# Performance work log

Hardware: AMD Instinct MI355X
Metric: run time of the kernel (lower is better)

The kernel has to match this reference:

```python
import jax, jax.numpy as jnp
import numpy as np

B, N, D = 4, 1024, 512
H, Dv, Dq = 8, 64, 64
NUM_BUCKETS = 64
LN_EPS = 1e-5


def setup_inputs() -> dict:
    key = jax.random.key(0)
    ks = jax.random.split(key, 10)
    x = jax.random.normal(ks[0], (B, N, D), dtype=jnp.float32)
    ts = jnp.sort(jax.random.randint(ks[1], (B, N), 0, 1_000_000), axis=1).astype(jnp.int64)
    cm = jnp.triu(jnp.ones((N, N), dtype=bool), k=1)  # causal: mask j > i
    pm = jnp.zeros((B, N), dtype=bool)                # no padding
    uvqk = 0.02 * jax.random.normal(ks[2], (D, 2 * H * Dv + 2 * H * Dq), dtype=jnp.float32)
    lim = float(np.sqrt(6.0 / (H * Dv + D)))
    o_w = jax.random.uniform(ks[3], (H * Dv, D), minval=-lim, maxval=lim, dtype=jnp.float32)
    o_b = jnp.zeros((D,), dtype=jnp.float32)
    ln_x_w = jnp.ones((D,), jnp.float32); ln_x_b = jnp.zeros((D,), jnp.float32)
    ln_a_w = jnp.ones((H * Dv,), jnp.float32); ln_a_b = jnp.zeros((H * Dv,), jnp.float32)
    ts_w = 0.02 * jax.random.normal(ks[4], (NUM_BUCKETS + 1,), dtype=jnp.float32)
    pos_w = 0.02 * jax.random.normal(ks[5], (2 * N - 1,), dtype=jnp.float32)
    return {"x": x, "ts": ts, "cm": cm, "pm": pm, "uvqk": uvqk, "o_w": o_w, "o_b": o_b,
            "ln_x_w": ln_x_w, "ln_x_b": ln_x_b, "ln_a_w": ln_a_w, "ln_a_b": ln_a_b,
            "ts_w": ts_w, "pos_w": pos_w}


def _layernorm(x, w, b):
    m = jnp.mean(x, axis=-1, keepdims=True)
    v = jnp.mean(jnp.square(x - m), axis=-1, keepdims=True)
    return (x - m) / jnp.sqrt(v + LN_EPS) * w + b


def _rel_bias(ts, ts_w, pos_w):
    # positional part: pb[i, j] = pos_w[j - i + N - 1], shape [N, N]
    idx = jnp.arange(N)
    pb = pos_w[idx[None, :] - idx[:, None] + N - 1]
    # bucketed time part
    ext = jnp.concatenate([ts, ts[:, N - 1:N]], axis=1)           # [B, N+1]
    diff = ext[:, 1:, None] - ext[:, None, :-1]                   # [B, N, N]
    logd = jnp.log(jnp.maximum(jnp.abs(diff), 1).astype(jnp.float32))
    bk = jnp.clip((logd / 0.301).astype(jnp.int32), 0, NUM_BUCKETS)
    return pb[None] + ts_w[bk]                                    # [B, N, N]


def reference(x, ts, cm, pm, uvqk, o_w, o_b, ln_x_w, ln_x_b, ln_a_w, ln_a_b, ts_w, pos_w):
    nx = _layernorm(x, ln_x_w, ln_x_b)                            # [B, N, D]
    out = jax.nn.silu(jnp.einsum('bnd,de->bne', nx, uvqk))        # [B, N, 2HDv+2HDq]
    u, v, q, k = jnp.split(out, [H * Dv, 2 * H * Dv, 2 * H * Dv + H * Dq], axis=-1)
    q = q.reshape(B, N, H, Dq)
    k = k.reshape(B, N, H, Dq)
    v = v.reshape(B, N, H, Dv)
    qk = jnp.einsum('bihd,bjhd->bhij', q, k) + _rel_bias(ts, ts_w, pos_w)[:, None]
    qk = jax.nn.silu(qk) / N
    qk = jnp.where(cm[None, None], 0.0, qk)          # causal mask
    qk = jnp.where(pm[:, None, None, :], 0.0, qk)    # padding mask on keys
    ao = jnp.einsum('bhij,bjhd->bihd', qk, v).reshape(B, N, H * Dv)
    ao = _layernorm(ao, ln_a_w, ln_a_b)
    u = u.reshape(B, N, H * Dv)
    y = (u * ao) @ o_w + o_b + x
    return jnp.where(pm[:, :, None], 0.0, y)
```

## Files before the change

### kernel.cpp

```cpp
#include <hip/hip_runtime.h>
#include <hip/hip_bf16.h>


typedef __attribute__((ext_vector_type(8))) short short8;
typedef __attribute__((ext_vector_type(4))) short bf4;
typedef __attribute__((ext_vector_type(4))) float floatx4;
typedef __attribute__((ext_vector_type(16))) float floatx16;

#define MFMA_BF16 __builtin_amdgcn_mfma_f32_16x16x32_bf16
#define MFMA32 __builtin_amdgcn_mfma_f32_32x32x16_bf16

static __device__ __forceinline__ short f2bf(float f) {
  unsigned u = __builtin_bit_cast(unsigned, f);
  u = (u + 0x7fffu + ((u >> 16) & 1u)) >> 16;
  return (short)u;
}
static __device__ __forceinline__ unsigned pk_bf16(float a, float b) {
  __hip_bfloat162 h = __float22bfloat162_rn(float2{a, b});
  unsigned u;
  __builtin_memcpy(&u, &h, 4);
  return u;
}
static __device__ __forceinline__ short lo16(unsigned u) { return (short)(u & 0xffffu); }
static __device__ __forceinline__ short hi16(unsigned u) { return (short)(u >> 16); }
static __device__ __forceinline__ float bf2f(short s) {
  unsigned u = ((unsigned)(unsigned short)s) << 16;
  return __builtin_bit_cast(float, u);
}
static __device__ __forceinline__ float bflo(unsigned u) {
  return __builtin_bit_cast(float, u << 16);
}
static __device__ __forceinline__ float bfhi(unsigned u) {
  return __builtin_bit_cast(float, u & 0xffff0000u);
}
static __device__ __forceinline__ float silu_f(float x) {
  return x / (1.f + __expf(-x));
}
static __device__ __forceinline__ void permswap(unsigned& a, unsigned& b) {
#if __has_builtin(__builtin_amdgcn_permlane32_swap)
  typedef __attribute__((ext_vector_type(2))) unsigned uint2v;
  uint2v r = __builtin_amdgcn_permlane32_swap(a, b, false, false);
  a = r[0];
  b = r[1];
#else
  asm volatile("v_permlane32_swap_b32 %0, %1" : "+v"(a), "+v"(b));
#endif
}
static __device__ __forceinline__ short8 mk8(unsigned a, unsigned b, unsigned c,
                                             unsigned d) {
  union {
    unsigned u[4];
    short8 s;
  } r;
  r.u[0] = a;
  r.u[1] = b;
  r.u[2] = c;
  r.u[3] = d;
  return r.s;
}
static __device__ __forceinline__ void gl_lds16(const void* g, void* l) {
  __builtin_amdgcn_global_load_lds(
      (const __attribute__((address_space(1))) unsigned int*)g,
      (__attribute__((address_space(3))) unsigned int*)l, 16, 0, 0);
}

__global__ __launch_bounds__(256) void prep_kernel(
    const float* __restrict__ x, const int* __restrict__ ts,
    const float* __restrict__ uvqk, const float* __restrict__ o_w,
    const float* __restrict__ ln_x_w, const float* __restrict__ ln_x_b,
    const float* __restrict__ ts_w, const float* __restrict__ pos_w,
    short* __restrict__ nx, short* __restrict__ uvqk_t,
    short* __restrict__ o_wt, short* __restrict__ bias) {
  __shared__ float tile[32][33];
  const int id = blockIdx.x;
  const int t = threadIdx.x;
  if (id < 4096) {
    const int b = id >> 10, i = id & 1023;
    int ie = i + 1; if (ie > 1023) ie = 1023;
    const int tse = ts[(b << 10) + ie];
    const int j0 = t * 4;
    int4 tj = *(const int4*)&ts[(b << 10) + j0];
    const int* tjp = (const int*)&tj;
    float ov[4];
#pragma unroll
    for (int e = 0; e < 4; ++e) {
      int dt = tse - tjp[e];
      float ad = fabsf((float)dt);
      if (ad < 1.f) ad = 1.f;
      int bkt = (int)(__logf(ad) * (1.f / 0.301f));
      if (bkt > 64) bkt = 64;
      ov[e] = pos_w[j0 + e - i + 1023] + ts_w[bkt];
    }
    uint2 o2 = {pk_bf16(ov[0], ov[1]), pk_bf16(ov[2], ov[3])};
    *(uint2*)&bias[((size_t)id << 10) + j0] = o2;
  } else if (id < 5120) {
    const int lane = t & 63;
    const int row = ((id - 4096) << 2) + (t >> 6);
    const int c0 = lane * 8;
    const float* xr = x + (size_t)row * 512;
    float v[8];
    *(float4*)&v[0] = *(const float4*)(xr + c0);
    *(float4*)&v[4] = *(const float4*)(xr + c0 + 4);
    float s = 0.f, sq = 0.f;
#pragma unroll
    for (int e = 0; e < 8; ++e) { s += v[e]; sq += v[e] * v[e]; }
#pragma unroll
    for (int off = 32; off > 0; off >>= 1) {
      s += __shfl_xor(s, off);
      sq += __shfl_xor(sq, off);
    }
    float m = s * (1.f / 512.f);
    float var = sq * (1.f / 512.f) - m * m;
    float rinv = rsqrtf(var + 1e-5f);
    float wv[8], bv[8];
    *(float4*)&wv[0] = *(const float4*)(ln_x_w + c0);
    *(float4*)&wv[4] = *(const float4*)(ln_x_w + c0 + 4);
    *(float4*)&bv[0] = *(const float4*)(ln_x_b + c0);
    *(float4*)&bv[4] = *(const float4*)(ln_x_b + c0 + 4);
    float o[8];
#pragma unroll
    for (int e = 0; e < 8; ++e) o[e] = (v[e] - m) * rinv * wv[e] + bv[e];
    uint4 o4 = {pk_bf16(o[0], o[1]), pk_bf16(o[2], o[3]),
                pk_bf16(o[4], o[5]), pk_bf16(o[6], o[7])};
    *(uint4*)(nx + (size_t)row * 512 + c0) = o4;
  } else {
    const float* src; short* dst; int R, C, bc, br;
    if (id < 6144) {
      int idm = id - 5120;
      src = uvqk; dst = uvqk_t; R = 512; C = 2048;
      bc = (idm & 63) * 32; br = (idm >> 6) * 32;
    } else {
      int idm = id - 6144;
      src = o_w; dst = o_wt; R = 512; C = 512;
      bc = (idm & 15) * 32; br = (idm >> 4) * 32;
    }
    const int c = t & 31, r0 = t >> 5;
#pragma unroll
    for (int p = 0; p < 4; ++p) {
      int r = r0 + p * 8;
      tile[r][c] = src[(size_t)(br + r) * C + bc + c];
    }
    __syncthreads();
#pragma unroll
    for (int p = 0; p < 4; ++p) {
      int r = r0 + p * 8;
      dst[(size_t)(bc + r) * R + br + c] = f2bf(tile[c][r]);
    }
  }
}

__global__ __launch_bounds__(256) void gemm1_kernel(
    const short* __restrict__ A, const short* __restrict__ Bt,
    short* __restrict__ u_buf, short* __restrict__ vt_buf,
    short* __restrict__ q_buf, short* __restrict__ k_buf) {
  __shared__ __align__(16) short As[2][128 * 32];
  __shared__ __align__(16) short Bs[2][128 * 32];
  const int t = threadIdx.x;
  const int lane = t & 63, w = t >> 6;
  const int quad = lane >> 4, l15 = lane & 15;
  const int m0 = blockIdx.x * 128, n0 = blockIdx.y * 128;
  const int wm = (w & 1) * 64, wn = (w >> 1) * 64;
  const int lr = lane >> 2, lc = (lane & 3) * 8;
  floatx4 acc[4][4];
#pragma unroll
  for (int i = 0; i < 4; ++i)
#pragma unroll
    for (int j = 0; j < 4; ++j) acc[i][j] = (floatx4){0.f, 0.f, 0.f, 0.f};

  for (int k0 = 0; k0 < 512; k0 += 64) {
    __syncthreads();
#pragma unroll
    for (int c = 0; c < 2; ++c)
#pragma unroll
      for (int p = 0; p < 2; ++p) {
        int ra = w * 32 + p * 16;
        gl_lds16(&A[(size_t)(m0 + ra + lr) * 512 + k0 + c * 32 + lc], &As[c][ra * 32]);
        gl_lds16(&Bt[(size_t)(n0 + ra + lr) * 512 + k0 + c * 32 + lc], &Bs[c][ra * 32]);
      }
    __syncthreads();
#pragma unroll
    for (int c = 0; c < 2; ++c) {
      short8 af[4], bfr[4];
#pragma unroll
      for (int mi = 0; mi < 4; ++mi) af[mi] = *(const short8*)&As[c][(wm + mi * 16 + l15) * 32 + quad * 8];
#pragma unroll
      for (int ni = 0; ni < 4; ++ni) bfr[ni] = *(const short8*)&Bs[c][(wn + ni * 16 + l15) * 32 + quad * 8];
#pragma unroll
      for (int mi = 0; mi < 4; ++mi)
#pragma unroll
        for (int ni = 0; ni < 4; ++ni)
          acc[mi][ni] = MFMA_BF16(af[mi], bfr[ni], acc[mi][ni], 0, 0, 0);
    }
  }
  const int seg = n0 >> 9, cbase = n0 & 511;
  if (seg == 0) {
#pragma unroll
    for (int mi = 0; mi < 4; ++mi)
#pragma unroll
      for (int ni = 0; ni < 4; ++ni) {
        int row0 = m0 + wm + mi * 16 + quad * 4;
        int c = cbase + wn + ni * 16 + l15;
        float v0 = silu_f(acc[mi][ni][0]), v1 = silu_f(acc[mi][ni][1]);
        float v2 = silu_f(acc[mi][ni][2]), v3 = silu_f(acc[mi][ni][3]);
        unsigned pa = pk_bf16(v0, v1), pb = pk_bf16(v2, v3);
        u_buf[(size_t)row0 * 512 + c] = lo16(pa);
        u_buf[(size_t)(row0 + 1) * 512 + c] = hi16(pa);
        u_buf[(size_t)(row0 + 2) * 512 + c] = lo16(pb);
        u_buf[(size_t)(row0 + 3) * 512 + c] = hi16(pb);
      }
  } else if (seg == 1) {
#pragma unroll
    for (int mi = 0; mi < 4; ++mi)
#pragma unroll
      for (int ni = 0; ni < 4; ++ni) {
        int c = cbase + wn + ni * 16 + l15;
        int h = c >> 6, d = c & 63;
        int row0 = m0 + wm + mi * 16 + quad * 4;
        int b_ = row0 >> 10, nb = row0 & 1023;
        float v0 = silu_f(acc[mi][ni][0]) * (1.f / 1024.f);
        float v1 = silu_f(acc[mi][ni][1]) * (1.f / 1024.f);
        float v2 = silu_f(acc[mi][ni][2]) * (1.f / 1024.f);
        float v3 = silu_f(acc[mi][ni][3]) * (1.f / 1024.f);
        uint2 sv = {pk_bf16(v0, v1), pk_bf16(v2, v3)};
        *(uint2*)&vt_buf[(((size_t)(b_ * 8 + h) * 64 + d) << 10) + nb] = sv;
      }
  } else {
    short* dst = (seg == 2) ? q_buf : k_buf;
#pragma unroll
    for (int mi = 0; mi < 4; ++mi)
#pragma unroll
      for (int ni = 0; ni < 4; ++ni) {
        int row0 = m0 + wm + mi * 16 + quad * 4;
        int c = cbase + wn + ni * 16 + l15;
        int b_ = row0 >> 10, nb = row0 & 1023;
        size_t base = ((((size_t)(b_ * 8 + (c >> 6))) << 10) + nb) * 64 + (c & 63);
        float v0 = silu_f(acc[mi][ni][0]), v1 = silu_f(acc[mi][ni][1]);
        float v2 = silu_f(acc[mi][ni][2]), v3 = silu_f(acc[mi][ni][3]);
        unsigned pa = pk_bf16(v0, v1), pb = pk_bf16(v2, v3);
        dst[base] = lo16(pa);
        dst[base + 64] = hi16(pa);
        dst[base + 128] = lo16(pb);
        dst[base + 192] = hi16(pb);
      }
  }
}

__global__ __launch_bounds__(256, 4) void attn_kernel(
    const short* __restrict__ q_buf, const short* __restrict__ k_buf,
    const short* __restrict__ vt_buf, const short* __restrict__ bias_buf,
    short* __restrict__ ao_part) {
  __shared__ __align__(16) short k_s[64][72];
  __shared__ __align__(16) short vt_s[64][72];
  __shared__ __align__(16) float red_s[2][32][64];

  const int t = threadIdx.x;
  const int lane = t & 63, w = t >> 6;
  const int l31 = lane & 31, hh = lane >> 5, h8 = hh * 8;
  const int wi = w & 1, wj = w >> 1;
  const int bh = blockIdx.x, pair = blockIdx.y, jh = blockIdx.z;
  const int b = bh >> 3, hd = bh & 7;
  const short* qh = q_buf + (size_t)bh * 65536;
  const short* kh = k_buf + (size_t)bh * 65536;
  const short* vth = vt_buf + (size_t)bh * 65536;
  const int sr = t >> 2, sc = (t & 3) * 16;

#pragma unroll
  for (int half = 0; half < 2; ++half) {
    const int it = half ? (15 - pair) : pair;
    const int i0 = it * 64;
    const int iw0 = i0 + wi * 32;
    const int ig = iw0 + l31;
    short8 qf[4];
#pragma unroll
    for (int kk = 0; kk < 4; ++kk)
      qf[kk] = *(const short8*)&qh[(size_t)ig * 64 + kk * 16 + h8];
    const short* brow = bias_buf + (((size_t)(b * 1024 + ig)) << 10);
    float4 kr0, kr1, vr0, vr1;
    {
      int j0 = jh * 64;
      kr0 = *(const float4*)&kh[(size_t)(j0 + sr) * 64 + sc];
      kr1 = *(const float4*)&kh[(size_t)(j0 + sr) * 64 + sc + 8];
      vr0 = *(const float4*)&vth[(size_t)sr * 1024 + j0 + sc];
      vr1 = *(const float4*)&vth[(size_t)sr * 1024 + j0 + sc + 8];
    }
    floatx16 ao0, ao1;
#pragma unroll
    for (int r = 0; r < 16; ++r) { ao0[r] = 0.f; ao1[r] = 0.f; }

    for (int jt = jh; jt <= it; jt += 4) {
      const int j0w = jt * 64 + wj * 32;
      const bool live = (j0w <= iw0 + 31);
      const bool needmask = live && (j0w + 31 > iw0);
      uint2 bw[4];
      if (live) {
#pragma unroll
        for (int g = 0; g < 4; ++g)
          bw[g] = *(const uint2*)&brow[j0w + g * 8 + hh * 4];
      }
      __syncthreads();
      *(float4*)&k_s[sr][sc] = kr0;
      *(float4*)&k_s[sr][sc + 8] = kr1;
      *(float4*)&vt_s[sr][sc] = vr0;
      *(float4*)&vt_s[sr][sc + 8] = vr1;
      {
        int jn = (jt + 4 <= it) ? jt + 4 : jt;
        int jn0 = jn * 64;
        kr0 = *(const float4*)&kh[(size_t)(jn0 + sr) * 64 + sc];
        kr1 = *(const float4*)&kh[(size_t)(jn0 + sr) * 64 + sc + 8];
        vr0 = *(const float4*)&vth[(size_t)sr * 1024 + jn0 + sc];
        vr1 = *(const float4*)&vth[(size_t)sr * 1024 + jn0 + sc + 8];
      }
      __syncthreads();
      if (!live) continue;
      __builtin_amdgcn_s_setprio(1);
      floatx16 s;
#pragma unroll
      for (int g = 0; g < 4; ++g) {
        s[4 * g + 0] = bflo(bw[g].x);
        s[4 * g + 1] = bfhi(bw[g].x);
        s[4 * g + 2] = bflo(bw[g].y);
        s[4 * g + 3] = bfhi(bw[g].y);
      }
#pragma unroll
      for (int kk = 0; kk < 4; ++kk) {
        short8 ak = *(const short8*)&k_s[wj * 32 + l31][kk * 16 + h8];
        s = MFMA32(ak, qf[kk], s, 0, 0, 0);
      }
      float p[16];
#pragma unroll
      for (int r = 0; r < 16; ++r) {
        float xv = s[r];
        float pv = xv / (1.f + __expf(-xv));
        if (needmask) {
          int jg = j0w + hh * 4 + (r & 3) + 8 * (r >> 2);
          if (jg > ig) pv = 0.f;
        }
        p[r] = pv;
      }
      unsigned X0 = pk_bf16(p[0], p[1]), Y0 = pk_bf16(p[2], p[3]);
      unsigned X1 = pk_bf16(p[4], p[5]), Y1 = pk_bf16(p[6], p[7]);
      unsigned X2 = pk_bf16(p[8], p[9]), Y2 = pk_bf16(p[10], p[11]);
      unsigned X3 = pk_bf16(p[12], p[13]), Y3 = pk_bf16(p[14], p[15]);
      permswap(X0, X1);
      permswap(Y0, Y1);
      permswap(X2, X3);
      permswap(Y2, Y3);
      short8 pa0 = mk8(X0, Y0, X1, Y1);
      short8 pa1 = mk8(X2, Y2, X3, Y3);
#pragma unroll
      for (int c = 0; c < 2; ++c) {
        short8 pa = c ? pa1 : pa0;
        short8 bv0 = *(const short8*)&vt_s[l31][wj * 32 + c * 16 + h8];
        short8 bv1 = *(const short8*)&vt_s[32 + l31][wj * 32 + c * 16 + h8];
        ao0 = MFMA32(pa, bv0, ao0, 0, 0, 0);
        ao1 = MFMA32(pa, bv1, ao1, 0, 0, 0);
      }
      __builtin_amdgcn_s_setprio(0);
    }
    __syncthreads();
    if (wj == 1) {
#pragma unroll
      for (int r = 0; r < 16; ++r) {
        int il = (r & 3) + 8 * (r >> 2) + 4 * hh;
        red_s[wi][il][l31] = ao0[r];
        red_s[wi][il][32 + l31] = ao1[r];
      }
    }
    __syncthreads();
    if (wj == 0) {
      short* aod = ao_part + (size_t)jh * 2097152;
#pragma unroll
      for (int r = 0; r < 16; ++r) {
        int il = (r & 3) + 8 * (r >> 2) + 4 * hh;
        float a0 = ao0[r] + red_s[wi][il][l31];
        float a1 = ao1[r] + red_s[wi][il][32 + l31];
        int gi = iw0 + il;
        size_t base = ((size_t)(b * 1024 + gi)) * 512 + hd * 64 + l31;
        aod[base] = f2bf(a0);
        aod[base + 32] = f2bf(a1);
      }
    }
  }
}

__global__ __launch_bounds__(256) void ln_mul_kernel(
    const short* __restrict__ ao_part, const short* __restrict__ u,
    const float* __restrict__ w_, const float* __restrict__ b_,
    short* __restrict__ g) {
  const int lane = threadIdx.x & 63;
  const int row = (blockIdx.x << 2) + (threadIdx.x >> 6);
  const int c0 = lane * 8;
  short8 a0 = *(const short8*)(ao_part + (size_t)row * 512 + c0);
  short8 a1 = *(const short8*)(ao_part + 2097152 + (size_t)row * 512 + c0);
  short8 a2 = *(const short8*)(ao_part + 4194304 + (size_t)row * 512 + c0);
  short8 a3 = *(const short8*)(ao_part + 6291456 + (size_t)row * 512 + c0);
  float v[8];
#pragma unroll
  for (int e = 0; e < 8; ++e)
    v[e] = (bf2f(a0[e]) + bf2f(a1[e])) + (bf2f(a2[e]) + bf2f(a3[e]));
  float s = 0.f, sq = 0.f;
#pragma unroll
  for (int e = 0; e < 8; ++e) { s += v[e]; sq += v[e] * v[e]; }
#pragma unroll
  for (int off = 32; off > 0; off >>= 1) {
    s += __shfl_xor(s, off);
    sq += __shfl_xor(sq, off);
  }
  float m = s * (1.f / 512.f);
  float var = sq * (1.f / 512.f) - m * m;
  float rinv = rsqrtf(var + 1e-5f);
  float wv[8], bv[8];
  *(float4*)&wv[0] = *(const float4*)(w_ + c0);
  *(float4*)&wv[4] = *(const float4*)(w_ + c0 + 4);
  *(float4*)&bv[0] = *(const float4*)(b_ + c0);
  *(float4*)&bv[4] = *(const float4*)(b_ + c0 + 4);
  short8 uv = *(const short8*)(u + (size_t)row * 512 + c0);
  float o[8];
#pragma unroll
  for (int e = 0; e < 8; ++e)
    o[e] = bf2f(uv[e]) * ((v[e] - m) * rinv * wv[e] + bv[e]);
  uint4 o4 = {pk_bf16(o[0], o[1]), pk_bf16(o[2], o[3]),
              pk_bf16(o[4], o[5]), pk_bf16(o[6], o[7])};
  *(uint4*)(g + (size_t)row * 512 + c0) = o4;
}

__global__ __launch_bounds__(256) void gemm2_kernel(
    const short* __restrict__ G, const short* __restrict__ Wt,
    const float* __restrict__ o_b, const float* __restrict__ x,
    float* __restrict__ out) {
  __shared__ __align__(16) short As[2][64 * 32];
  __shared__ __align__(16) short Bs[2][64 * 32];
  const int t = threadIdx.x;
  const int lane = t & 63, w = t >> 6;
  const int quad = lane >> 4, l15 = lane & 15;
  const int m0 = blockIdx.x * 64, n0 = blockIdx.y * 64;
  const int lr = lane >> 2, lc = (lane & 3) * 8;
  floatx4 acc[4];
#pragma unroll
  for (int j = 0; j < 4; ++j) acc[j] = (floatx4){0.f, 0.f, 0.f, 0.f};

  for (int k0 = 0; k0 < 512; k0 += 64) {
    __syncthreads();
#pragma unroll
    for (int c = 0; c < 2; ++c) {
      int ra = w * 16;
      gl_lds16(&G[(size_t)(m0 + ra + lr) * 512 + k0 + c * 32 + lc], &As[c][ra * 32]);
      gl_lds16(&Wt[(size_t)(n0 + ra + lr) * 512 + k0 + c * 32 + lc], &Bs[c][ra * 32]);
    }
    __syncthreads();
#pragma unroll
    for (int c = 0; c < 2; ++c) {
      short8 af = *(const short8*)&As[c][(w * 16 + l15) * 32 + quad * 8];
#pragma unroll
      for (int ni = 0; ni < 4; ++ni) {
        short8 bfr = *(const short8*)&Bs[c][(ni * 16 + l15) * 32 + quad * 8];
        acc[ni] = MFMA_BF16(af, bfr, acc[ni], 0, 0, 0);
      }
    }
  }
#pragma unroll
  for (int ni = 0; ni < 4; ++ni)
#pragma unroll
    for (int r = 0; r < 4; ++r) {
      int row = m0 + w * 16 + quad * 4 + r;
      int c = n0 + ni * 16 + l15;
      out[(size_t)row * 512 + c] = acc[ni][r] + o_b[c] + x[(size_t)row * 512 + c];
    }
}

extern "C" void kernel_launch(void* const* d_in, const int* in_sizes, int n_in,
                              void* d_out, int out_size, void* d_ws, size_t ws_size,
                              hipStream_t stream) {
  const float* x = (const float*)d_in[0];
  const int* ts = (const int*)d_in[1];
  const float* uvqk = (const float*)d_in[4];
  const float* o_w = (const float*)d_in[5];
  const float* o_b = (const float*)d_in[6];
  const float* ln_x_w = (const float*)d_in[7];
  const float* ln_x_b = (const float*)d_in[8];
  const float* ln_a_w = (const float*)d_in[9];
  const float* ln_a_b = (const float*)d_in[10];
  const float* ts_w = (const float*)d_in[11];
  const float* pos_w = (const float*)d_in[12];
  float* out = (float*)d_out;

  char* ws = (char*)d_ws;
  short* nx = (short*)(ws + 0);
  short* uvqk_t = (short*)(ws + 4194304);
  short* o_wt = (short*)(ws + 6291456);
  short* u_buf = (short*)(ws + 6815744);
  short* q_buf = (short*)(ws + 11010048);
  short* k_buf = (short*)(ws + 15204352);
  short* vt_buf = (short*)(ws + 19398656);
  short* bias_buf = (short*)(ws + 23592960);
  short* ao_part = (short*)(ws + 31981568);
  short* g_buf = nx;

  hipLaunchKernelGGL(prep_kernel, dim3(6400), dim3(256), 0, stream,
                     x, ts, uvqk, o_w, ln_x_w, ln_x_b, ts_w, pos_w,
                     nx, uvqk_t, o_wt, bias_buf);
  hipLaunchKernelGGL(gemm1_kernel, dim3(32, 16), dim3(256), 0, stream, nx, uvqk_t, u_buf, vt_buf, q_buf, k_buf);
  hipLaunchKernelGGL(attn_kernel, dim3(32, 8, 4), dim3(256), 0, stream, q_buf, k_buf, vt_buf, bias_buf, ao_part);
  hipLaunchKernelGGL(ln_mul_kernel, dim3(1024), dim3(256), 0, stream, ao_part, u_buf, ln_a_w, ln_a_b, g_buf);
  hipLaunchKernelGGL(gemm2_kernel, dim3(64, 8), dim3(256), 0, stream, g_buf, o_wt, o_b, x, out);
}
```

Baseline: 144.5 us.

## Compute relative bias on the fly inside attention instead of materializing it

Result: slower. 160.6 us (+11.1%).

```diff
diff --git a/kernel.cpp b/kernel.cpp
--- a/kernel.cpp
+++ b/kernel.cpp
@@ -26,12 +26,6 @@
 static __device__ __forceinline__ float bf2f(short s) {
   unsigned u = ((unsigned)(unsigned short)s) << 16;
   return __builtin_bit_cast(float, u);
-}
-static __device__ __forceinline__ float bflo(unsigned u) {
-  return __builtin_bit_cast(float, u << 16);
-}
-static __device__ __forceinline__ float bfhi(unsigned u) {
-  return __builtin_bit_cast(float, u & 0xffff0000u);
 }
 static __device__ __forceinline__ float silu_f(float x) {
   return x / (1.f + __expf(-x));
@@ -65,37 +59,17 @@
 }
 
 __global__ __launch_bounds__(256) void prep_kernel(
-    const float* __restrict__ x, const int* __restrict__ ts,
+    const float* __restrict__ x,
     const float* __restrict__ uvqk, const float* __restrict__ o_w,
     const float* __restrict__ ln_x_w, const float* __restrict__ ln_x_b,
-    const float* __restrict__ ts_w, const float* __restrict__ pos_w,
     short* __restrict__ nx, short* __restrict__ uvqk_t,
-    short* __restrict__ o_wt, short* __restrict__ bias) {
+    short* __restrict__ o_wt) {
   __shared__ float tile[32][33];
   const int id = blockIdx.x;
   const int t = threadIdx.x;
-  if (id < 4096) {
-    const int b = id >> 10, i = id & 1023;
-    int ie = i + 1; if (ie > 1023) ie = 1023;
-    const int tse = ts[(b << 10) + ie];
-    const int j0 = t * 4;
-    int4 tj = *(const int4*)&ts[(b << 10) + j0];
-    const int* tjp = (const int*)&tj;
-    float ov[4];
-#pragma unroll
-    for (int e = 0; e < 4; ++e) {
-      int dt = tse - tjp[e];
-      float ad = fabsf((float)dt);
-      if (ad < 1.f) ad = 1.f;
-      int bkt = (int)(__logf(ad) * (1.f / 0.301f));
-      if (bkt > 64) bkt = 64;
-      ov[e] = pos_w[j0 + e - i + 1023] + ts_w[bkt];
-    }
-    uint2 o2 = {pk_bf16(ov[0], ov[1]), pk_bf16(ov[2], ov[3])};
-    *(uint2*)&bias[((size_t)id << 10) + j0] = o2;
-  } else if (id < 5120) {
+  if (id < 1024) {
     const int lane = t & 63;
-    const int row = ((id - 4096) << 2) + (t >> 6);
+    const int row = (id << 2) + (t >> 6);
     const int c0 = lane * 8;
     const float* xr = x + (size_t)row * 512;
     float v[8];
@@ -125,12 +99,12 @@
     *(uint4*)(nx + (size_t)row * 512 + c0) = o4;
   } else {
     const float* src; short* dst; int R, C, bc, br;
-    if (id < 6144) {
-      int idm = id - 5120;
+    if (id < 2048) {
+      int idm = id - 1024;
       src = uvqk; dst = uvqk_t; R = 512; C = 2048;
       bc = (idm & 63) * 32; br = (idm >> 6) * 32;
     } else {
-      int idm = id - 6144;
+      int idm = id - 2048;
       src = o_w; dst = o_wt; R = 512; C = 512;
       bc = (idm & 15) * 32; br = (idm >> 4) * 32;
     }
@@ -247,7 +221,8 @@
 
 __global__ __launch_bounds__(256, 4) void attn_kernel(
     const short* __restrict__ q_buf, const short* __restrict__ k_buf,
-    const short* __restrict__ vt_buf, const short* __restrict__ bias_buf,
+    const short* __restrict__ vt_buf, const int* __restrict__ ts,
+    const float* __restrict__ ts_w, const float* __restrict__ pos_w,
     short* __restrict__ ao_part) {
   __shared__ __align__(16) short k_s[64][72];
   __shared__ __align__(16) short vt_s[64][72];
@@ -262,6 +237,7 @@
   const short* qh = q_buf + (size_t)bh * 65536;
   const short* kh = k_buf + (size_t)bh * 65536;
   const short* vth = vt_buf + (size_t)bh * 65536;
+  const int* ts_b = ts + (b << 10);
   const int sr = t >> 2, sc = (t & 3) * 16;
 
 #pragma unroll
@@ -270,11 +246,12 @@
     const int i0 = it * 64;
     const int iw0 = i0 + wi * 32;
     const int ig = iw0 + l31;
+    const int tse = ts_b[(ig + 1 <= 1023) ? ig + 1 : 1023];
+    const float* pw = pos_w + 1023 - ig;
     short8 qf[4];
 #pragma unroll
     for (int kk = 0; kk < 4; ++kk)
       qf[kk] = *(const short8*)&qh[(size_t)ig * 64 + kk * 16 + h8];
-    const short* brow = bias_buf + (((size_t)(b * 1024 + ig)) << 10);
     float4 kr0, kr1, vr0, vr1;
     {
       int j0 = jh * 64;
@@ -291,11 +268,18 @@
       const int j0w = jt * 64 + wj * 32;
       const bool live = (j0w <= iw0 + 31);
       const bool needmask = live && (j0w + 31 > iw0);
-      uint2 bw[4];
+      float bi[16];
       if (live) {
 #pragma unroll
-        for (int g = 0; g < 4; ++g)
-          bw[g] = *(const uint2*)&brow[j0w + g * 8 + hh * 4];
+        for (int r = 0; r < 16; ++r) {
+          int jg = j0w + hh * 4 + (r & 3) + 8 * (r >> 2);
+          int dt = tse - ts_b[jg];
+          float ad = fabsf((float)dt);
+          if (ad < 1.f) ad = 1.f;
+          int bkt = (int)(__logf(ad) * (1.f / 0.301f));
+          if (bkt > 64) bkt = 64;
+          bi[r] = pw[jg] + ts_w[bkt];
+        }
       }
       __syncthreads();
       *(float4*)&k_s[sr][sc] = kr0;
@@ -315,12 +299,7 @@
       __builtin_amdgcn_s_setprio(1);
       floatx16 s;
 #pragma unroll
-      for (int g = 0; g < 4; ++g) {
-        s[4 * g + 0] = bflo(bw[g].x);
-        s[4 * g + 1] = bfhi(bw[g].x);
-        s[4 * g + 2] = bflo(bw[g].y);
-        s[4 * g + 3] = bfhi(bw[g].y);
-      }
+      for (int r = 0; r < 16; ++r) s[r] = bi[r];
 #pragma unroll
       for (int kk = 0; kk < 4; ++kk) {
         short8 ak = *(const short8*)&k_s[wj * 32 + l31][kk * 16 + h8];
@@ -492,15 +471,13 @@
   short* q_buf = (short*)(ws + 11010048);
   short* k_buf = (short*)(ws + 15204352);
   short* vt_buf = (short*)(ws + 19398656);
-  short* bias_buf = (short*)(ws + 23592960);
   short* ao_part = (short*)(ws + 31981568);
   short* g_buf = nx;
 
-  hipLaunchKernelGGL(prep_kernel, dim3(6400), dim3(256), 0, stream,
-                     x, ts, uvqk, o_w, ln_x_w, ln_x_b, ts_w, pos_w,
-                     nx, uvqk_t, o_wt, bias_buf);
+  hipLaunchKernelGGL(prep_kernel, dim3(2304), dim3(256), 0, stream,
+                     x, uvqk, o_w, ln_x_w, ln_x_b, nx, uvqk_t, o_wt);
   hipLaunchKernelGGL(gemm1_kernel, dim3(32, 16), dim3(256), 0, stream, nx, uvqk_t, u_buf, vt_buf, q_buf, k_buf);
-  hipLaunchKernelGGL(attn_kernel, dim3(32, 8, 4), dim3(256), 0, stream, q_buf, k_buf, vt_buf, bias_buf, ao_part);
+  hipLaunchKernelGGL(attn_kernel, dim3(32, 8, 4), dim3(256), 0, stream, q_buf, k_buf, vt_buf, ts, ts_w, pos_w, ao_part);
   hipLaunchKernelGGL(ln_mul_kernel, dim3(1024), dim3(256), 0, stream, ao_part, u_buf, ln_a_w, ln_a_b, g_buf);
   hipLaunchKernelGGL(gemm2_kernel, dim3(64, 8), dim3(256), 0, stream, g_buf, o_wt, o_b, x, out);
 }
```
